# Optimization experiments

Hardware: AMD Instinct MI355X
Metric: run time of the kernel (lower is better)

## Reference

```python
import jax, jax.numpy as jnp
import numpy as np
from jax import lax

B, T, CIN, COUT, FACTOR = 2, 2048, 512, 512, 2
KUP = FACTOR * 2          # transposed-conv kernel
PUP = FACTOR // 2         # transposed-conv padding
KR, PR = 7, 3             # refine conv kernel/padding
EPS = 1e-5


def _ste(x, q):
    # straight-through estimator: forward = q, backward = identity
    return x + lax.stop_gradient(q - x)


def act_quant(x):
    # BitNet b1.58 per-token int8 absmax quant; x is (B, C, L), quant over C
    scale = 127.0 / jnp.maximum(jnp.max(jnp.abs(x), axis=1, keepdims=True), 1e-5)
    q = jnp.clip(jnp.round(x * scale), -128, 127) / scale
    return _ste(x, q)


def weight_quant(w):
    # ternary {-1,0,1} * scale, scale = mean |w|
    scale = 1.0 / jnp.maximum(jnp.mean(jnp.abs(w)), 1e-5)
    q = jnp.clip(jnp.round(w * scale), -1, 1) / scale
    return _ste(w, q)


def bit_conv1d(x, w, b, pad):
    # x: (B,C,L), w: (Cout,Cin,K) torch layout
    y = lax.conv_general_dilated(
        act_quant(x), weight_quant(w), window_strides=(1,),
        padding=[(pad, pad)], dimension_numbers=('NCH', 'OIH', 'NCH'))
    return y + b[None, :, None]


def bit_conv_transpose1d(x, w, b, stride, pad):
    # x: (B,Cin,L), w: (Cin,Cout,K) torch ConvTranspose1d layout
    k = w.shape[2]
    y = lax.conv_general_dilated(
        act_quant(x), jnp.flip(weight_quant(w), 2), window_strides=(1,),
        padding=[(k - 1 - pad, k - 1 - pad)], lhs_dilation=(stride,),
        dimension_numbers=('NCH', 'IOH', 'NCH'))
    return y + b[None, :, None]


def setup_inputs() -> dict:
    key = jax.random.key(0)
    ks = jax.random.split(key, 7)
    s_up = 1.0 / np.sqrt(CIN * KUP)
    s_r = 1.0 / np.sqrt(COUT * KR)
    return {
        'x': jax.random.normal(ks[0], (B, T, CIN), jnp.float32),
        'w_up': jax.random.normal(ks[1], (CIN, COUT, KUP), jnp.float32) * s_up,
        'b_up': jnp.zeros((COUT,), jnp.float32),
        'w_r1': jax.random.normal(ks[2], (COUT, COUT, KR), jnp.float32) * s_r,
        'b_r1': jnp.zeros((COUT,), jnp.float32),
        'w_r2': jax.random.normal(ks[3], (COUT, COUT, KR), jnp.float32) * s_r,
        'b_r2': jnp.zeros((COUT,), jnp.float32),
        'ln_w': jnp.ones((COUT,), jnp.float32),
        'ln_b': jnp.zeros((COUT,), jnp.float32),
    }


def reference(x, w_up, b_up, w_r1, b_r1, w_r2, b_r2, ln_w, ln_b):
    h = jnp.swapaxes(x, 1, 2)                                  # (B,Cin,T)
    h = bit_conv_transpose1d(h, w_up, b_up, FACTOR, PUP)       # (B,Cout,factor*T)
    r = bit_conv1d(h, w_r1, b_r1, PR)
    r = jax.nn.silu(r)
    r = bit_conv1d(r, w_r2, b_r2, PR)
    h = h + r
    h = jnp.swapaxes(h, 1, 2)                                  # (B,L,Cout)
    mu = jnp.mean(h, axis=-1, keepdims=True)
    var = jnp.mean(jnp.square(h - mu), axis=-1, keepdims=True)
    return (h - mu) * lax.rsqrt(var + EPS) * ln_w + ln_b
```

## Files before the change

kernel.cpp:

```cpp
#include <hip/hip_runtime.h>
#include <hip/hip_bf16.h>
#include <cstdint>
#include <cstddef>


#define B_ 2
#define T_ 2048
#define L_ 4096
#define C_ 512

static constexpr int NUP = 512 * 512 * 4;
static constexpr int NR  = 512 * 512 * 7;

using v4i  = __attribute__((ext_vector_type(4))) int;
using v16i = __attribute__((ext_vector_type(16))) int;

__device__ __forceinline__ void gl16(const void* g, void* l) {
  __builtin_amdgcn_global_load_lds((const __attribute__((address_space(1))) unsigned int*)g,
                                   (__attribute__((address_space(3))) unsigned int*)l,
                                   16, 0, 0);
}


__device__ inline float block_reduce_sum_256(float v) {
  #pragma unroll
  for (int off = 32; off > 0; off >>= 1) v += __shfl_down(v, off, 64);
  __shared__ float s[4];
  __syncthreads();
  if ((threadIdx.x & 63) == 0) s[threadIdx.x >> 6] = v;
  __syncthreads();
  return (s[0] + s[1]) + (s[2] + s[3]);
}

__global__ void abssum3_kernel(const float* __restrict__ w0, const float* __restrict__ w1,
                               const float* __restrict__ w2, float* __restrict__ out) {
  int y = blockIdx.y;
  const float* w = (y == 0) ? w0 : (y == 1) ? w1 : w2;
  int n = (y == 0) ? NUP : NR;
  int idx = blockIdx.x * 256 + threadIdx.x;
  float s = 0.f;
  for (int i = idx; i < n; i += gridDim.x * 256) s += fabsf(w[i]);
  s = block_reduce_sum_256(s);
  if (threadIdx.x == 0) atomicAdd(out + y, s);
}

__global__ void tern_all_kernel(const float* __restrict__ wu, const float* __restrict__ w1,
                                const float* __restrict__ w2, int8_t* __restrict__ ou,
                                int8_t* __restrict__ o1, int8_t* __restrict__ o2,
                                const float* __restrict__ wsum) {
  int y = blockIdx.y;
  int idx = blockIdx.x * 256 + threadIdx.x;
  if (y == 0) {
    if (idx >= NUP) return;
    float mean = wsum[0] * (1.0f / (float)NUP);
    float scale = 1.0f / fmaxf(mean, 1e-5f);
    float t = rintf(wu[idx] * scale);
    t = fminf(fmaxf(t, -1.f), 1.f);
    int ci = idx >> 11;
    int co = (idx >> 2) & 511;
    int k = idx & 3;
    int ptap = (k == 3) ? 0 : (k == 1) ? 1 : (k == 2) ? 2 : 3;
    ou[(((size_t)ptap * 32 + (ci >> 4)) * 512 + co) * 16 + (ci & 15)] = (int8_t)t;
  } else {
    if (idx >= NR) return;
    const float* w = (y == 1) ? w1 : w2;
    int8_t* o = (y == 1) ? o1 : o2;
    float mean = wsum[y] * (1.0f / (float)NR);
    float scale = 1.0f / fmaxf(mean, 1e-5f);
    float t = rintf(w[idx] * scale);
    t = fminf(fmaxf(t, -1.f), 1.f);
    int co = idx / 3584;
    int rem = idx - co * 3584;
    int ci = rem / 7;
    int k = rem - ci * 7;
    o[(((size_t)k * 32 + (ci >> 4)) * 512 + co) * 16 + (ci & 15)] = (int8_t)t;
  }
}

__global__ void act_quant_kernel(const float* __restrict__ x, int8_t* __restrict__ qd,
                                 float* __restrict__ inv, int Lb, int lbsh, int LinH) {
  int tok = blockIdx.x;
  int b = tok >> lbsh;
  int t = tok & (Lb - 1);
  const float* row = x + (size_t)tok * C_;
  int tid = threadIdx.x;
  float v0 = row[tid];
  float v1 = row[tid + 256];
  float m = fmaxf(fabsf(v0), fabsf(v1));
  #pragma unroll
  for (int off = 32; off > 0; off >>= 1) m = fmaxf(m, __shfl_down(m, off, 64));
  __shared__ float s[4];
  __shared__ __align__(16) int8_t sq[512];
  if ((tid & 63) == 0) s[tid >> 6] = m;
  __syncthreads();
  m = fmaxf(fmaxf(s[0], s[1]), fmaxf(s[2], s[3]));
  float scale = 127.0f / fmaxf(m, 1e-5f);
  float q0 = fminf(fmaxf(rintf(v0 * scale), -128.f), 127.f);
  float q1 = fminf(fmaxf(rintf(v1 * scale), -128.f), 127.f);
  sq[tid] = (int8_t)q0;
  sq[tid + 256] = (int8_t)q1;
  __syncthreads();
  if (tid < 32)
    *(v4i*)(qd + ((size_t)(b * 32 + tid) * LinH + 8 + t) * 16) = *(const v4i*)(sq + tid * 16);
  if (tid == 0) inv[(size_t)b * LinH + 8 + t] = 1.0f / scale;
}

template<int NTAPS, bool CONVT>
__global__ __launch_bounds__(256)
void conv_mfma(const int8_t* __restrict__ qin, const float* __restrict__ invp, int LinH,
               const int8_t* __restrict__ wq, const float* __restrict__ wsum, int widx,
               float wninv, const float* __restrict__ bias, const float* __restrict__ res,
               float* __restrict__ outp, int Lout, int do_silu) {
  __shared__ __align__(16) int8_t sA[32 * 70 * 16];
  __shared__ __align__(16) int8_t sB[2][8 * 128 * 16];
  __shared__ float sInv[72];

  const int tid = threadIdx.x;
  const int w = tid >> 6, lane = tid & 63, q = lane >> 5, l31 = lane & 31;
  const int mh = w & 1, nh = w >> 1;
  const int n0 = (blockIdx.x & 3) * 128;
  const int t0 = (blockIdx.x >> 2) * 64;
  const int b = blockIdx.y;
  int s0 = -3;
  const int8_t* wq_p = wq;
  float* out_b = outp + (size_t)b * Lout * 512;
  int rstride = 512;
  if (CONVT) {
    int parity = blockIdx.z;
    s0 = parity - 1;
    wq_p += (size_t)parity * 2 * 32 * 512 * 16;
    out_b += parity * 512;
    rstride = 1024;
  }
  const int8_t* qin_b = qin + (size_t)b * 32 * LinH * 16;
  const float* inv_b = invp + (size_t)b * LinH + 8;

  auto stageB = [&](int j, int buf) {
    int tap = j >> 2, kc = j & 3;
    const int8_t* wt = wq_p + ((size_t)(tap * 32 + kc * 8) * 512 + n0) * 16;
    #pragma unroll
    for (int i = 0; i < 4; ++i) {
      int u = i * 256 + tid;
      gl16(wt + ((size_t)(u >> 7) * 512 + (u & 127)) * 16,
           sB[buf] + (size_t)(i * 256 + w * 64) * 16);
    }
  };

  stageB(0, 0);
  #pragma unroll
  for (int i = 0; i < 9; ++i) {
    int base = i * 256 + w * 64;
    if (base < 2240) {
      int u = base + lane;
      int kq = u / 70;
      int row = u - kq * 70;
      gl16(qin_b + ((size_t)kq * LinH + (size_t)(t0 + 5 + row)) * 16,
           sA + (size_t)base * 16);
    }
  }
  if (tid < 70) sInv[tid] = inv_b[t0 - 3 + tid];
  __syncthreads();

  float fs0[16], fs1[16];
  v16i acc0{}, acc1{};
  #pragma unroll
  for (int r = 0; r < 16; ++r) { fs0[r] = 0.f; fs1[r] = 0.f; acc0[r] = 0; acc1[r] = 0; }

  constexpr int NCH = NTAPS * 4;

  auto doChunk = [&](int j, int cur) {
    const int tap = j >> 2, kc = j & 3;
    const int shift = s0 + tap;
    if (j + 1 < NCH) stageB(j + 1, cur ^ 1);
    const int arow = 3 + shift + mh * 32 + l31;
    #pragma unroll
    for (int s = 0; s < 4; ++s) {
      int kqc = s * 2 + q;
      v4i a  = *(const v4i*)(sA + ((size_t)((kc * 8 + kqc) * 70) + arow) * 16);
      v4i b0 = *(const v4i*)(sB[cur] + ((size_t)kqc * 128 + nh * 64 + l31) * 16);
      v4i b1 = *(const v4i*)(sB[cur] + ((size_t)kqc * 128 + nh * 64 + 32 + l31) * 16);
      acc0 = __builtin_amdgcn_mfma_i32_32x32x32_i8(a, b0, acc0, 0, 0, 0);
      acc1 = __builtin_amdgcn_mfma_i32_32x32x32_i8(a, b1, acc1, 0, 0, 0);
    }
    if (kc == 3) {
      #pragma unroll
      for (int r = 0; r < 16; ++r) {
        int ro = (r & 3) + 8 * (r >> 2) + 4 * q;
        float sc = sInv[3 + shift + mh * 32 + ro];
        fs0[r] = fmaf((float)acc0[r], sc, fs0[r]);
        fs1[r] = fmaf((float)acc1[r], sc, fs1[r]);
        acc0[r] = 0;
        acc1[r] = 0;
      }
    }
    __syncthreads();
  };

  #pragma unroll 1
  for (int j = 0; j < NCH; j += 2) {
    doChunk(j, 0);
    doChunk(j + 1, 1);
  }

  float wdq = fmaxf(wsum[widx] * wninv, 1e-5f);
  #pragma unroll
  for (int nt = 0; nt < 2; ++nt) {
    int col = n0 + nh * 64 + nt * 32 + l31;
    float bv = bias[col];
    #pragma unroll
    for (int r = 0; r < 16; ++r) {
      int row = t0 + mh * 32 + (r & 3) + 8 * (r >> 2) + 4 * q;
      float y = (nt == 0 ? fs0[r] : fs1[r]) * wdq + bv;
      if (do_silu) y = y / (1.0f + expf(-y));
      if (res) y += res[((size_t)b * Lout + row) * 512 + col];
      out_b[(size_t)row * rstride + col] = y;
    }
  }
}

__global__ void ln_kernel(const float* __restrict__ x, const float* __restrict__ g,
                          const float* __restrict__ be, float* __restrict__ out) {
  int tok = blockIdx.x;
  const float* row = x + (size_t)tok * C_;
  int tid = threadIdx.x;
  float v0 = row[tid];
  float v1 = row[tid + 256];
  float total = block_reduce_sum_256(v0 + v1);
  float mu = total * (1.0f / (float)C_);
  float d0 = v0 - mu, d1 = v1 - mu;
  float vs = block_reduce_sum_256(d0 * d0 + d1 * d1);
  float var = vs * (1.0f / (float)C_);
  float r = 1.0f / sqrtf(var + 1e-5f);
  size_t base = (size_t)tok * C_;
  out[base + tid] = d0 * r * g[tid] + be[tid];
  out[base + tid + 256] = d1 * r * g[tid + 256] + be[tid + 256];
}


extern "C" void kernel_launch(void* const* d_in, const int* in_sizes, int n_in,
                              void* d_out, int out_size, void* d_ws, size_t ws_size,
                              hipStream_t stream) {
  const float* x    = (const float*)d_in[0];
  const float* w_up = (const float*)d_in[1];
  const float* b_up = (const float*)d_in[2];
  const float* w_r1 = (const float*)d_in[3];
  const float* b_r1 = (const float*)d_in[4];
  const float* w_r2 = (const float*)d_in[5];
  const float* b_r2 = (const float*)d_in[6];
  const float* ln_w = (const float*)d_in[7];
  const float* ln_b = (const float*)d_in[8];
  float* out = (float*)d_out;

  const int LXH = T_ + 16;
  const int LHH = L_ + 16;

  char* ws = (char*)d_ws;
  size_t off = 0;
  auto alloc = [&](size_t sz) { size_t p = off; off += (sz + 255) & ~(size_t)255; return p; };
  float*  wsum = (float*) (ws + alloc(256));
  int8_t* qx   = (int8_t*)(ws + alloc((size_t)B_ * 32 * LXH * 16));
  int8_t* qh   = (int8_t*)(ws + alloc((size_t)B_ * 32 * LHH * 16));
  size_t zero_bytes = off;
  float*  invx = (float*) (ws + alloc((size_t)B_ * LXH * 4));
  float*  invh = (float*) (ws + alloc((size_t)B_ * LHH * 4));
  int8_t* wqup = (int8_t*)(ws + alloc((size_t)4 * 32 * 512 * 16));
  int8_t* wq1  = (int8_t*)(ws + alloc((size_t)7 * 32 * 512 * 16));
  int8_t* wq2  = (int8_t*)(ws + alloc((size_t)7 * 32 * 512 * 16));
  float*  h    = (float*) (ws + alloc((size_t)B_ * L_ * C_ * 4));
  float*  r    = (float*) (ws + alloc((size_t)B_ * L_ * C_ * 4));

  hipMemsetAsync(ws, 0, zero_bytes, stream);

  abssum3_kernel<<<dim3(256, 3), 256, 0, stream>>>(w_up, w_r1, w_r2, wsum);
  tern_all_kernel<<<dim3(NR / 256, 3), 256, 0, stream>>>(w_up, w_r1, w_r2,
                                                         wqup, wq1, wq2, wsum);

  act_quant_kernel<<<B_ * T_, 256, 0, stream>>>(x, qx, invx, T_, 11, LXH);

  conv_mfma<2, true><<<dim3(4 * 32, B_, 2), 256, 0, stream>>>(
      qx, invx, LXH, wqup, wsum, 0, 1.0f / (float)NUP, b_up, nullptr, h, L_, 0);

  act_quant_kernel<<<B_ * L_, 256, 0, stream>>>(h, qh, invh, L_, 12, LHH);

  conv_mfma<7, false><<<dim3(4 * 64, B_, 1), 256, 0, stream>>>(
      qh, invh, LHH, wq1, wsum, 1, 1.0f / (float)NR, b_r1, nullptr, r, L_, 1);

  act_quant_kernel<<<B_ * L_, 256, 0, stream>>>(r, qh, invh, L_, 12, LHH);

  conv_mfma<7, false><<<dim3(4 * 64, B_, 1), 256, 0, stream>>>(
      qh, invh, LHH, wq2, wsum, 2, 1.0f / (float)NR, b_r2, h, r, L_, 0);

  ln_kernel<<<B_ * L_, 256, 0, stream>>>(r, ln_w, ln_b, out);
}
```

Before: 214.1 us.

## Deepen weight staging to a 4-buffer pipeline with fine-grained vmcnt waits

Splits each K-chunk of weights into halves and stages them into four LDS buffers, prefetching three chunks ahead. The full __syncthreads per chunk is replaced by an explicit s_waitcnt vmcnt followed by s_barrier, so global loads issued earlier can stay in flight while the MFMAs run. The aim is to hide global-to-LDS latency for the weights. The cost is twice as many barrier iterations with less MFMA work each, and the correctness of the hand-written waitcnt counts and the reuse of the sA and sInv loads depends on the order in which loads are issued.

```diff
diff --git a/kernel.cpp b/kernel.cpp
--- a/kernel.cpp
+++ b/kernel.cpp
@@ -112,7 +112,7 @@
                float wninv, const float* __restrict__ bias, const float* __restrict__ res,
                float* __restrict__ outp, int Lout, int do_silu) {
   __shared__ __align__(16) int8_t sA[32 * 70 * 16];
-  __shared__ __align__(16) int8_t sB[2][8 * 128 * 16];
+  __shared__ __align__(16) int8_t sB[4][4 * 128 * 16];
   __shared__ float sInv[72];
 
   const int tid = threadIdx.x;
@@ -135,18 +135,22 @@
   const int8_t* qin_b = qin + (size_t)b * 32 * LinH * 16;
   const float* inv_b = invp + (size_t)b * LinH + 8;
 
+  constexpr int NCH = NTAPS * 8;
+
   auto stageB = [&](int j, int buf) {
-    int tap = j >> 2, kc = j & 3;
-    const int8_t* wt = wq_p + ((size_t)(tap * 32 + kc * 8) * 512 + n0) * 16;
+    int tap = j >> 3, kc = j & 7;
+    const int8_t* wt = wq_p + ((size_t)((tap * 32 + kc * 4) * 512) + n0) * 16;
+    int8_t* dst = (int8_t*)sB[buf];
     #pragma unroll
-    for (int i = 0; i < 4; ++i) {
-      int u = i * 256 + tid;
-      gl16(wt + ((size_t)(u >> 7) * 512 + (u & 127)) * 16,
-           sB[buf] + (size_t)(i * 256 + w * 64) * 16);
+    for (int i = 0; i < 2; ++i) {
+      int ub = i * 256 + w * 64;
+      int u = ub + lane;
+      gl16(wt + ((size_t)(u >> 7) * 512 + (u & 127)) * 16, dst + (size_t)ub * 16);
     }
   };
 
-  stageB(0, 0);
+  float iv = 0.f;
+  if (tid < 70) iv = inv_b[t0 - 3 + tid];
   #pragma unroll
   for (int i = 0; i < 9; ++i) {
     int base = i * 256 + w * 64;
@@ -158,31 +162,38 @@
            sA + (size_t)base * 16);
     }
   }
-  if (tid < 70) sInv[tid] = inv_b[t0 - 3 + tid];
-  __syncthreads();
+  stageB(0, 0);
+  stageB(1, 1);
+  stageB(2, 2);
+  if (tid < 70) sInv[tid] = iv;
+  asm volatile("s_waitcnt lgkmcnt(0)" ::: "memory");
 
   float fs0[16], fs1[16];
   v16i acc0{}, acc1{};
   #pragma unroll
   for (int r = 0; r < 16; ++r) { fs0[r] = 0.f; fs1[r] = 0.f; acc0[r] = 0; acc1[r] = 0; }
 
-  constexpr int NCH = NTAPS * 4;
-
-  auto doChunk = [&](int j, int cur) {
-    const int tap = j >> 2, kc = j & 3;
+  auto doIter = [&](int j, int wmode) {
+    if (wmode == 0)      asm volatile("s_waitcnt vmcnt(4)" ::: "memory");
+    else if (wmode == 1) asm volatile("s_waitcnt vmcnt(2)" ::: "memory");
+    else                 asm volatile("s_waitcnt vmcnt(0)" ::: "memory");
+    __builtin_amdgcn_s_barrier();
+    if (j + 3 < NCH) stageB(j + 3, (j + 3) & 3);
+    const int tap = j >> 3, kc = j & 7;
     const int shift = s0 + tap;
-    if (j + 1 < NCH) stageB(j + 1, cur ^ 1);
     const int arow = 3 + shift + mh * 32 + l31;
+    const int8_t* bufp = (const int8_t*)sB[j & 3];
     #pragma unroll
-    for (int s = 0; s < 4; ++s) {
-      int kqc = s * 2 + q;
-      v4i a  = *(const v4i*)(sA + ((size_t)((kc * 8 + kqc) * 70) + arow) * 16);
-      v4i b0 = *(const v4i*)(sB[cur] + ((size_t)kqc * 128 + nh * 64 + l31) * 16);
-      v4i b1 = *(const v4i*)(sB[cur] + ((size_t)kqc * 128 + nh * 64 + 32 + l31) * 16);
+    for (int s = 0; s < 2; ++s) {
+      int kql = s * 2 + q;
+      int kq = kc * 4 + kql;
+      v4i a  = *(const v4i*)(sA + ((size_t)(kq * 70) + arow) * 16);
+      v4i b0 = *(const v4i*)(bufp + ((size_t)kql * 128 + nh * 64 + l31) * 16);
+      v4i b1 = *(const v4i*)(bufp + ((size_t)kql * 128 + nh * 64 + 32 + l31) * 16);
       acc0 = __builtin_amdgcn_mfma_i32_32x32x32_i8(a, b0, acc0, 0, 0, 0);
       acc1 = __builtin_amdgcn_mfma_i32_32x32x32_i8(a, b1, acc1, 0, 0, 0);
     }
-    if (kc == 3) {
+    if ((j & 7) == 7) {
       #pragma unroll
       for (int r = 0; r < 16; ++r) {
         int ro = (r & 3) + 8 * (r >> 2) + 4 * q;
@@ -193,14 +204,12 @@
         acc1[r] = 0;
       }
     }
-    __syncthreads();
   };
 
   #pragma unroll 1
-  for (int j = 0; j < NCH; j += 2) {
-    doChunk(j, 0);
-    doChunk(j + 1, 1);
-  }
+  for (int j = 0; j < NCH - 2; ++j) doIter(j, 0);
+  doIter(NCH - 2, 1);
+  doIter(NCH - 1, 2);
 
   float wdq = fmaxf(wsum[widx] * wninv, 1e-5f);
   #pragma unroll
```

Result: slower. 258.4 us (+20.7%).

## Load conv weights directly from global memory and widen block tile to 64x256

Applied to the files above, without the earlier changes.

Removes the LDS double-buffered staging of ternary weights and the per-chunk barriers, having each wave read its weight fragments directly from global/L2. Each block now covers 256 output channels, with each wave computing a 64x64 tile via four MFMA accumulators, so the grid is halved. This trades LDS traffic and synchronisation for exposed global-load latency and higher register pressure with one block per CU.

```diff
diff --git a/kernel.cpp b/kernel.cpp
--- a/kernel.cpp
+++ b/kernel.cpp
@@ -106,20 +106,18 @@
 }
 
 template<int NTAPS, bool CONVT>
-__global__ __launch_bounds__(256)
+__global__ __launch_bounds__(256, 1)
 void conv_mfma(const int8_t* __restrict__ qin, const float* __restrict__ invp, int LinH,
                const int8_t* __restrict__ wq, const float* __restrict__ wsum, int widx,
                float wninv, const float* __restrict__ bias, const float* __restrict__ res,
                float* __restrict__ outp, int Lout, int do_silu) {
   __shared__ __align__(16) int8_t sA[32 * 70 * 16];
-  __shared__ __align__(16) int8_t sB[2][8 * 128 * 16];
   __shared__ float sInv[72];
 
   const int tid = threadIdx.x;
   const int w = tid >> 6, lane = tid & 63, q = lane >> 5, l31 = lane & 31;
-  const int mh = w & 1, nh = w >> 1;
-  const int n0 = (blockIdx.x & 3) * 128;
-  const int t0 = (blockIdx.x >> 2) * 64;
+  const int n0 = (blockIdx.x & 1) * 256;
+  const int t0 = (blockIdx.x >> 1) * 64;
   const int b = blockIdx.y;
   int s0 = -3;
   const int8_t* wq_p = wq;
@@ -135,18 +133,6 @@
   const int8_t* qin_b = qin + (size_t)b * 32 * LinH * 16;
   const float* inv_b = invp + (size_t)b * LinH + 8;
 
-  auto stageB = [&](int j, int buf) {
-    int tap = j >> 2, kc = j & 3;
-    const int8_t* wt = wq_p + ((size_t)(tap * 32 + kc * 8) * 512 + n0) * 16;
-    #pragma unroll
-    for (int i = 0; i < 4; ++i) {
-      int u = i * 256 + tid;
-      gl16(wt + ((size_t)(u >> 7) * 512 + (u & 127)) * 16,
-           sB[buf] + (size_t)(i * 256 + w * 64) * 16);
-    }
-  };
-
-  stageB(0, 0);
   #pragma unroll
   for (int i = 0; i < 9; ++i) {
     int base = i * 256 + w * 64;
@@ -161,59 +147,61 @@
   if (tid < 70) sInv[tid] = inv_b[t0 - 3 + tid];
   __syncthreads();
 
-  float fs0[16], fs1[16];
-  v16i acc0{}, acc1{};
-  #pragma unroll
-  for (int r = 0; r < 16; ++r) { fs0[r] = 0.f; fs1[r] = 0.f; acc0[r] = 0; acc1[r] = 0; }
-
-  constexpr int NCH = NTAPS * 4;
-
-  auto doChunk = [&](int j, int cur) {
-    const int tap = j >> 2, kc = j & 3;
+  float fs00[16], fs01[16], fs10[16], fs11[16];
+  v16i acc00{}, acc01{}, acc10{}, acc11{};
+  #pragma unroll
+  for (int r = 0; r < 16; ++r) { fs00[r] = 0.f; fs01[r] = 0.f; fs10[r] = 0.f; fs11[r] = 0.f; }
+
+  const int8_t* wt_base = wq_p + ((size_t)q * 512 + (size_t)(n0 + w * 64 + l31)) * 16;
+
+  #pragma unroll 1
+  for (int tap = 0; tap < NTAPS; ++tap) {
     const int shift = s0 + tap;
-    if (j + 1 < NCH) stageB(j + 1, cur ^ 1);
-    const int arow = 3 + shift + mh * 32 + l31;
+    const int arow0 = 3 + shift + l31;
+    const int8_t* wt = wt_base + (size_t)tap * 32 * 512 * 16;
+    const int8_t* aB = sA + ((size_t)q * 70 + arow0) * 16;
     #pragma unroll
-    for (int s = 0; s < 4; ++s) {
-      int kqc = s * 2 + q;
-      v4i a  = *(const v4i*)(sA + ((size_t)((kc * 8 + kqc) * 70) + arow) * 16);
-      v4i b0 = *(const v4i*)(sB[cur] + ((size_t)kqc * 128 + nh * 64 + l31) * 16);
-      v4i b1 = *(const v4i*)(sB[cur] + ((size_t)kqc * 128 + nh * 64 + 32 + l31) * 16);
-      acc0 = __builtin_amdgcn_mfma_i32_32x32x32_i8(a, b0, acc0, 0, 0, 0);
-      acc1 = __builtin_amdgcn_mfma_i32_32x32x32_i8(a, b1, acc1, 0, 0, 0);
-    }
-    if (kc == 3) {
+    for (int ks = 0; ks < 16; ++ks) {
+      const int kq = ks * 2;
+      v4i a0 = *(const v4i*)(aB + (size_t)kq * 70 * 16);
+      v4i a1 = *(const v4i*)(aB + ((size_t)kq * 70 + 32) * 16);
+      v4i b0 = *(const v4i*)(wt + (size_t)kq * 512 * 16);
+      v4i b1 = *(const v4i*)(wt + ((size_t)kq * 512 + 32) * 16);
+      acc00 = __builtin_amdgcn_mfma_i32_32x32x32_i8(a0, b0, acc00, 0, 0, 0);
+      acc01 = __builtin_amdgcn_mfma_i32_32x32x32_i8(a0, b1, acc01, 0, 0, 0);
+      acc10 = __builtin_amdgcn_mfma_i32_32x32x32_i8(a1, b0, acc10, 0, 0, 0);
+      acc11 = __builtin_amdgcn_mfma_i32_32x32x32_i8(a1, b1, acc11, 0, 0, 0);
+    }
+    #pragma unroll
+    for (int r = 0; r < 16; ++r) {
+      int ro = (r & 3) + 8 * (r >> 2) + 4 * q;
+      float sc0 = sInv[3 + shift + ro];
+      float sc1 = sInv[3 + shift + 32 + ro];
+      fs00[r] = fmaf((float)acc00[r], sc0, fs00[r]);
+      fs01[r] = fmaf((float)acc01[r], sc0, fs01[r]);
+      fs10[r] = fmaf((float)acc10[r], sc1, fs10[r]);
+      fs11[r] = fmaf((float)acc11[r], sc1, fs11[r]);
+      acc00[r] = 0; acc01[r] = 0; acc10[r] = 0; acc11[r] = 0;
+    }
+  }
+
+  float wdq = fmaxf(wsum[widx] * wninv, 1e-5f);
+  #pragma unroll
+  for (int mrep = 0; mrep < 2; ++mrep) {
+    #pragma unroll
+    for (int nt = 0; nt < 2; ++nt) {
+      int col = n0 + w * 64 + nt * 32 + l31;
+      float bv = bias[col];
       #pragma unroll
       for (int r = 0; r < 16; ++r) {
-        int ro = (r & 3) + 8 * (r >> 2) + 4 * q;
-        float sc = sInv[3 + shift + mh * 32 + ro];
-        fs0[r] = fmaf((float)acc0[r], sc, fs0[r]);
-        fs1[r] = fmaf((float)acc1[r], sc, fs1[r]);
-        acc0[r] = 0;
-        acc1[r] = 0;
+        int row = t0 + mrep * 32 + (r & 3) + 8 * (r >> 2) + 4 * q;
+        float v = (mrep == 0) ? (nt == 0 ? fs00[r] : fs01[r])
+                              : (nt == 0 ? fs10[r] : fs11[r]);
+        float y = v * wdq + bv;
+        if (do_silu) y = y / (1.0f + expf(-y));
+        if (res) y += res[((size_t)b * Lout + row) * 512 + col];
+        out_b[(size_t)row * rstride + col] = y;
       }
-    }
-    __syncthreads();
-  };
-
-  #pragma unroll 1
-  for (int j = 0; j < NCH; j += 2) {
-    doChunk(j, 0);
-    doChunk(j + 1, 1);
-  }
-
-  float wdq = fmaxf(wsum[widx] * wninv, 1e-5f);
-  #pragma unroll
-  for (int nt = 0; nt < 2; ++nt) {
-    int col = n0 + nh * 64 + nt * 32 + l31;
-    float bv = bias[col];
-    #pragma unroll
-    for (int r = 0; r < 16; ++r) {
-      int row = t0 + mh * 32 + (r & 3) + 8 * (r >> 2) + 4 * q;
-      float y = (nt == 0 ? fs0[r] : fs1[r]) * wdq + bv;
-      if (do_silu) y = y / (1.0f + expf(-y));
-      if (res) y += res[((size_t)b * Lout + row) * 512 + col];
-      out_b[(size_t)row * rstride + col] = y;
     }
   }
 }
@@ -277,17 +265,17 @@
 
   act_quant_kernel<<<B_ * T_, 256, 0, stream>>>(x, qx, invx, T_, 11, LXH);
 
-  conv_mfma<2, true><<<dim3(4 * 32, B_, 2), 256, 0, stream>>>(
+  conv_mfma<2, true><<<dim3(2 * 32, B_, 2), 256, 0, stream>>>(
       qx, invx, LXH, wqup, wsum, 0, 1.0f / (float)NUP, b_up, nullptr, h, L_, 0);
 
   act_quant_kernel<<<B_ * L_, 256, 0, stream>>>(h, qh, invh, L_, 12, LHH);
 
-  conv_mfma<7, false><<<dim3(4 * 64, B_, 1), 256, 0, stream>>>(
+  conv_mfma<7, false><<<dim3(2 * 64, B_, 1), 256, 0, stream>>>(
       qh, invh, LHH, wq1, wsum, 1, 1.0f / (float)NR, b_r1, nullptr, r, L_, 1);
 
   act_quant_kernel<<<B_ * L_, 256, 0, stream>>>(r, qh, invh, L_, 12, LHH);
 
-  conv_mfma<7, false><<<dim3(4 * 64, B_, 1), 256, 0, stream>>>(
+  conv_mfma<7, false><<<dim3(2 * 64, B_, 1), 256, 0, stream>>>(
       qh, invh, LHH, wq2, wsum, 2, 1.0f / (float)NR, b_r2, h, r, L_, 0);
 
   ln_kernel<<<B_ * L_, 256, 0, stream>>>(r, ln_w, ln_b, out);
```

Result: slower. 275.3 us (+28.6%).
